# Kernel optimization log

Hardware: AMD Instinct MI355X
Metric: run time of the kernel (lower is better)

## Reference

```python
import jax, jax.numpy as jnp
import numpy as np

N_QUBITS = 22


def setup_inputs() -> dict:
    n = N_QUBITS
    dim = 2 ** n
    key = jax.random.key(0)
    k1, k2, k3, k4, k5 = jax.random.split(key, 5)
    return {
        "state_real": jax.random.normal(k1, (dim,), jnp.float32),
        "state_imag": jax.random.normal(k2, (dim,), jnp.float32),
        "rabi": jax.random.uniform(k3, (1,), jnp.float32),
        "detune": jax.random.uniform(k4, (1,), jnp.float32),
        "U": jax.random.normal(k5, (n, n), jnp.float32),
        "n_qubits": n,
    }


def reference(state_real, state_imag, rabi, detune, U, n_qubits):
    """kron_sum of H_rabi (Pauli-X per qubit, weight rabi/2), diagonal detune
    (weight -detune per qubit) and diagonal pairwise interaction (triu(U,1)),
    applied to a 2**n complex state vector."""
    n = n_qubits
    dim = 2 ** n
    psi = (state_real + 1j * state_imag).astype(jnp.complex64).reshape((2,) * n)

    # parse_weights: per-qubit rabi/2 for X terms, -detune for number operators
    w_x = jnp.full((n,), rabi[0] * 0.5)
    w_d = jnp.full((n,), -detune[0])

    # sum_k (rabi/2) * X_k |psi>  : X_k flips qubit-k axis of the state tensor
    x_acc = jnp.zeros_like(psi)
    for k in range(n):  # fixed small structural loop over qubits
        x_acc = x_acc + w_x[k] * jnp.flip(psi, axis=k)

    # bit table: bits[k, b] = k-th qubit bit of basis index b (axis 0 = MSB)
    basis = jnp.arange(dim, dtype=jnp.uint32)
    shifts = jnp.arange(n - 1, -1, -1, dtype=jnp.uint32)
    bits = ((basis[None, :] >> shifts[:, None]) & 1).astype(jnp.float32)  # [n, 2**n]

    # diagonal one-body detune: sum_k w_d[k] * bit_k
    diag_one = jnp.einsum("k,kn->n", w_d, bits)
    # diagonal two-body interaction: sum_{i<j} U[i,j] * bit_i * bit_j
    Ut = jnp.triu(U, k=1)
    diag_two = jnp.sum((Ut @ bits) * bits, axis=0)

    diag = (diag_one + diag_two).reshape((2,) * n)
    out = (x_acc + diag * psi).reshape(dim)
    return jnp.stack([out.real, out.imag])  # [2, 2**n] (real, imag)
```

## Files before the change

kernel.cpp:

```cpp
#include <hip/hip_runtime.h>

#define NQ 22
#define DIM (1 << NQ)
#define TILE 2048
#define LOG_TILE 11

typedef float f32x4_t __attribute__((ext_vector_type(4)));

__global__ __launch_bounds__(256) void ryd_precompute_B(const float* __restrict__ U,
                                                        float* __restrict__ Btab) {
    int t = blockIdx.x * blockDim.x + threadIdx.x;
    __shared__ float Us[NQ * NQ];
    for (int i = threadIdx.x; i < NQ * NQ; i += blockDim.x) Us[i] = U[i];
    __syncthreads();
    float b = 0.f;
    #pragma unroll
    for (int p = 1; p <= 10; ++p) {
        if ((t >> p) & 1) {
            #pragma unroll
            for (int q = 0; q < p; ++q) {
                if ((t >> q) & 1) b += Us[(21 - p) * NQ + (21 - q)];
            }
        }
    }
    Btab[t] = b;
}

#define ACC8(a0, a1, b0, b1)                                              \
    do {                                                                  \
        ar[0] += (a0).x; ar[1] += (a0).y; ar[2] += (a0).z; ar[3] += (a0).w; \
        ar[4] += (a1).x; ar[5] += (a1).y; ar[6] += (a1).z; ar[7] += (a1).w; \
        ai[0] += (b0).x; ai[1] += (b0).y; ai[2] += (b0).z; ai[3] += (b0).w; \
        ai[4] += (b1).x; ai[5] += (b1).y; ai[6] += (b1).z; ai[7] += (b1).w; \
    } while (0)

__device__ __forceinline__ int swz(int c) { return c ^ ((c >> 3) & 1); }

__global__ __launch_bounds__(256) void ryd_rows(
    const float* __restrict__ sr_g, const float* __restrict__ si_g,
    const float* __restrict__ rabi, const float* __restrict__ detune,
    const float* __restrict__ U, const float* __restrict__ Btab,
    float* __restrict__ out) {
    __shared__ float4 srv[TILE / 4];
    __shared__ float4 siv[TILE / 4];
    __shared__ float AD[12];

    const int h = blockIdx.x;
    const int tid = threadIdx.x;
    const int m0 = tid << 3;
    const int base = h << LOG_TILE;

    float4 r0 = *(const float4*)(sr_g + base + m0);
    float4 r1 = *(const float4*)(sr_g + base + m0 + 4);
    float4 i0 = *(const float4*)(si_g + base + m0);
    float4 i1 = *(const float4*)(si_g + base + m0 + 4);

    float4 B0 = *(const float4*)(Btab + m0);
    float4 B1 = *(const float4*)(Btab + m0 + 4);

    srv[swz(2 * tid)]     = r0;
    srv[swz(2 * tid + 1)] = r1;
    siv[swz(2 * tid)]     = i0;
    siv[swz(2 * tid + 1)] = i1;

    if (tid < 11) {
        int q = tid;
        float d = 0.f;
        #pragma unroll
        for (int hp = 0; hp <= 10; ++hp)
            if ((h >> hp) & 1) d += U[(10 - hp) * NQ + (21 - q)];
        AD[q] = d;
    } else if (tid == 11) {
        float a = 0.f;
        #pragma unroll
        for (int hp = 1; hp <= 10; ++hp) {
            if ((h >> hp) & 1) {
                #pragma unroll
                for (int hq = 0; hq < hp; ++hq)
                    if ((h >> hq) & 1) a += U[(10 - hp) * NQ + (10 - hq)];
            }
        }
        AD[11] = a;
    }

    float pr[8]  = {r0.x, r0.y, r0.z, r0.w, r1.x, r1.y, r1.z, r1.w};
    float pi_[8] = {i0.x, i0.y, i0.z, i0.w, i1.x, i1.y, i1.z, i1.w};

    __syncthreads();

    float ar[8], ai[8];
    #pragma unroll
    for (int e = 0; e < 8; ++e) {
        ar[e] = pr[e ^ 1] + pr[e ^ 2] + pr[e ^ 4];
        ai[e] = pi_[e ^ 1] + pi_[e ^ 2] + pi_[e ^ 4];
    }

    #pragma unroll
    for (int jj = 0; jj < 8; ++jj) {
        int p = tid ^ (1 << jj);
        float4 a0 = srv[swz(2 * p)];
        float4 a1 = srv[swz(2 * p + 1)];
        float4 b0 = siv[swz(2 * p)];
        float4 b1 = siv[swz(2 * p + 1)];
        ACC8(a0, a1, b0, b1);
    }

    const float det = detune[0];
    const float hrabi = 0.5f * rabi[0];
    float Dq0 = AD[0] - det;
    float Dq1 = AD[1] - det;
    float Dq2 = AD[2] - det;
    float diagBase = AD[11] - det * (float)__popc((unsigned)h);
    #pragma unroll
    for (int j = 0; j < 8; ++j)
        if ((tid >> j) & 1) diagBase += AD[j + 3] - det;

    float Bv[8] = {B0.x, B0.y, B0.z, B0.w, B1.x, B1.y, B1.z, B1.w};

    float orv[8], oiv[8];
    #pragma unroll
    for (int e = 0; e < 8; ++e) {
        float d = diagBase + Bv[e];
        if (e & 1) d += Dq0;
        if (e & 2) d += Dq1;
        if (e & 4) d += Dq2;
        orv[e] = hrabi * ar[e] + d * pr[e];
        oiv[e] = hrabi * ai[e] + d * pi_[e];
    }

    f32x4_t o0 = {orv[0], orv[1], orv[2], orv[3]};
    f32x4_t o1 = {orv[4], orv[5], orv[6], orv[7]};
    f32x4_t o2 = {oiv[0], oiv[1], oiv[2], oiv[3]};
    f32x4_t o3 = {oiv[4], oiv[5], oiv[6], oiv[7]};
    __builtin_nontemporal_store(o0, (f32x4_t*)(out + base + m0));
    __builtin_nontemporal_store(o1, (f32x4_t*)(out + base + m0 + 4));
    __builtin_nontemporal_store(o2, (f32x4_t*)(out + DIM + base + m0));
    __builtin_nontemporal_store(o3, (f32x4_t*)(out + DIM + base + m0 + 4));
}

__global__ __launch_bounds__(1024, 4) void ryd_cols(
    const float* __restrict__ sr_g, const float* __restrict__ si_g,
    const float* __restrict__ rabi, float* __restrict__ out) {
    __shared__ f32x4_t L[TILE * 4];

    const int b = blockIdx.x;
    const int A = b & 1;
    const int C0 = (b >> 1) << 4;
    const float* __restrict__ src = A ? si_g : sr_g;
    float* __restrict__ dst = out + (A ? DIM : 0);
    const int t = threadIdx.x;
    const float hrabi = 0.5f * rabi[0];

    #pragma unroll
    for (int k = 0; k < 8; ++k) {
        int n = t + (k << 10);
        int r = n >> 2, cv = n & 3;
        L[(r << 2) + cv] = *(const f32x4_t*)(src + (r << 11) + C0 + (cv << 2));
    }

    f32x4_t cur[8];
    #pragma unroll
    for (int k = 0; k < 8; ++k) {
        int n = t + (k << 10);
        int r = n >> 2, cv = n & 3;
        cur[k] = __builtin_nontemporal_load(
            (const f32x4_t*)(dst + (r << 11) + C0 + (cv << 2)));
    }

    __syncthreads();

    #pragma unroll
    for (int k = 0; k < 8; ++k) {
        int n = t + (k << 10);
        int r = n >> 2, cv = n & 3;
        f32x4_t acc = L[((r ^ 1) << 2) + cv];
        #pragma unroll
        for (int j = 1; j < 11; ++j)
            acc += L[(((r ^ (1 << j)) << 2)) + cv];
        f32x4_t res = cur[k] + acc * hrabi;
        __builtin_nontemporal_store(res, (f32x4_t*)(dst + (r << 11) + C0 + (cv << 2)));
    }
}

extern "C" void kernel_launch(void* const* d_in, const int* in_sizes, int n_in,
                              void* d_out, int out_size, void* d_ws, size_t ws_size,
                              hipStream_t stream) {
    const float* state_real = (const float*)d_in[0];
    const float* state_imag = (const float*)d_in[1];
    const float* rabi       = (const float*)d_in[2];
    const float* detune     = (const float*)d_in[3];
    const float* U          = (const float*)d_in[4];
    float* Btab = (float*)d_ws;
    float* out  = (float*)d_out;

    ryd_precompute_B<<<TILE / 256, 256, 0, stream>>>(U, Btab);
    ryd_rows<<<DIM / TILE, 256, 0, stream>>>(state_real, state_imag, rabi, detune,
                                             U, Btab, out);
    ryd_cols<<<256, 1024, 0, stream>>>(state_real, state_imag, rabi, out);
}
```

Before: 132.6 us.

## Run column-flip pass first with half-height tiles, then accumulate in row pass

The column kernel (high-qubit flips) now runs before the row kernel and writes partial results. The row kernel reads those partials and adds its own terms. Each column block covers only 1024 rows, taking the top-bit partner directly from global memory, which doubles the block count and halves shared memory per block. This aims to raise occupancy and parallelism in the column pass at the cost of extra global reads of the partner half-tile.

```diff
diff --git a/kernel.cpp b/kernel.cpp
--- a/kernel.cpp
+++ b/kernel.cpp
@@ -35,6 +35,53 @@
     } while (0)
 
 __device__ __forceinline__ int swz(int c) { return c ^ ((c >> 3) & 1); }
+
+__global__ __launch_bounds__(512, 4) void ryd_cols(
+    const float* __restrict__ sr_g, const float* __restrict__ si_g,
+    const float* __restrict__ rabi, float* __restrict__ out) {
+    __shared__ f32x4_t L[1024 * 4];
+
+    const int b = blockIdx.x;
+    const int A = b & 1;
+    const int half = (b >> 1) & 1;
+    const int C0 = (b >> 2) << 4;
+    const int R0 = half << 10;
+    const float* __restrict__ src = A ? si_g : sr_g;
+    float* __restrict__ dst = out + (A ? DIM : 0);
+    const int t = threadIdx.x;
+    const float hrabi = 0.5f * rabi[0];
+
+    #pragma unroll
+    for (int k = 0; k < 8; ++k) {
+        int n = t + (k << 9);
+        int r = n >> 2, cv = n & 3;
+        L[(r << 2) + cv] =
+            *(const f32x4_t*)(src + ((R0 + r) << 11) + C0 + (cv << 2));
+    }
+
+    f32x4_t pp[8];
+    #pragma unroll
+    for (int k = 0; k < 8; ++k) {
+        int n = t + (k << 9);
+        int r = n >> 2, cv = n & 3;
+        pp[k] = *(const f32x4_t*)(src + (((R0 ^ 1024) + r) << 11) + C0 + (cv << 2));
+    }
+
+    __syncthreads();
+
+    #pragma unroll
+    for (int k = 0; k < 8; ++k) {
+        int n = t + (k << 9);
+        int r = n >> 2, cv = n & 3;
+        f32x4_t acc = pp[k];
+        #pragma unroll
+        for (int j = 0; j < 10; ++j)
+            acc += L[((r ^ (1 << j)) << 2) + cv];
+        f32x4_t res = acc * hrabi;
+        __builtin_nontemporal_store(
+            res, (f32x4_t*)(dst + ((R0 + r) << 11) + C0 + (cv << 2)));
+    }
+}
 
 __global__ __launch_bounds__(256) void ryd_rows(
     const float* __restrict__ sr_g, const float* __restrict__ si_g,
@@ -57,6 +104,11 @@
 
     float4 B0 = *(const float4*)(Btab + m0);
     float4 B1 = *(const float4*)(Btab + m0 + 4);
+
+    float4 z0 = *(const float4*)(out + base + m0);
+    float4 z1 = *(const float4*)(out + base + m0 + 4);
+    float4 z2 = *(const float4*)(out + DIM + base + m0);
+    float4 z3 = *(const float4*)(out + DIM + base + m0 + 4);
 
     srv[swz(2 * tid)]     = r0;
     srv[swz(2 * tid + 1)] = r1;
@@ -116,6 +168,8 @@
         if ((tid >> j) & 1) diagBase += AD[j + 3] - det;
 
     float Bv[8] = {B0.x, B0.y, B0.z, B0.w, B1.x, B1.y, B1.z, B1.w};
+    float zr[8] = {z0.x, z0.y, z0.z, z0.w, z1.x, z1.y, z1.z, z1.w};
+    float zi[8] = {z2.x, z2.y, z2.z, z2.w, z3.x, z3.y, z3.z, z3.w};
 
     float orv[8], oiv[8];
     #pragma unroll
@@ -124,8 +178,8 @@
         if (e & 1) d += Dq0;
         if (e & 2) d += Dq1;
         if (e & 4) d += Dq2;
-        orv[e] = hrabi * ar[e] + d * pr[e];
-        oiv[e] = hrabi * ai[e] + d * pi_[e];
+        orv[e] = zr[e] + hrabi * ar[e] + d * pr[e];
+        oiv[e] = zi[e] + hrabi * ai[e] + d * pi_[e];
     }
 
     f32x4_t o0 = {orv[0], orv[1], orv[2], orv[3]};
@@ -136,50 +190,6 @@
     __builtin_nontemporal_store(o1, (f32x4_t*)(out + base + m0 + 4));
     __builtin_nontemporal_store(o2, (f32x4_t*)(out + DIM + base + m0));
     __builtin_nontemporal_store(o3, (f32x4_t*)(out + DIM + base + m0 + 4));
-}
-
-__global__ __launch_bounds__(1024, 4) void ryd_cols(
-    const float* __restrict__ sr_g, const float* __restrict__ si_g,
-    const float* __restrict__ rabi, float* __restrict__ out) {
-    __shared__ f32x4_t L[TILE * 4];
-
-    const int b = blockIdx.x;
-    const int A = b & 1;
-    const int C0 = (b >> 1) << 4;
-    const float* __restrict__ src = A ? si_g : sr_g;
-    float* __restrict__ dst = out + (A ? DIM : 0);
-    const int t = threadIdx.x;
-    const float hrabi = 0.5f * rabi[0];
-
-    #pragma unroll
-    for (int k = 0; k < 8; ++k) {
-        int n = t + (k << 10);
-        int r = n >> 2, cv = n & 3;
-        L[(r << 2) + cv] = *(const f32x4_t*)(src + (r << 11) + C0 + (cv << 2));
-    }
-
-    f32x4_t cur[8];
-    #pragma unroll
-    for (int k = 0; k < 8; ++k) {
-        int n = t + (k << 10);
-        int r = n >> 2, cv = n & 3;
-        cur[k] = __builtin_nontemporal_load(
-            (const f32x4_t*)(dst + (r << 11) + C0 + (cv << 2)));
-    }
-
-    __syncthreads();
-
-    #pragma unroll
-    for (int k = 0; k < 8; ++k) {
-        int n = t + (k << 10);
-        int r = n >> 2, cv = n & 3;
-        f32x4_t acc = L[((r ^ 1) << 2) + cv];
-        #pragma unroll
-        for (int j = 1; j < 11; ++j)
-            acc += L[(((r ^ (1 << j)) << 2)) + cv];
-        f32x4_t res = cur[k] + acc * hrabi;
-        __builtin_nontemporal_store(res, (f32x4_t*)(dst + (r << 11) + C0 + (cv << 2)));
-    }
 }
 
 extern "C" void kernel_launch(void* const* d_in, const int* in_sizes, int n_in,
@@ -194,7 +204,7 @@
     float* out  = (float*)d_out;
 
     ryd_precompute_B<<<TILE / 256, 256, 0, stream>>>(U, Btab);
+    ryd_cols<<<512, 512, 0, stream>>>(state_real, state_imag, rabi, out);
     ryd_rows<<<DIM / TILE, 256, 0, stream>>>(state_real, state_imag, rabi, detune,
                                              U, Btab, out);
-    ryd_cols<<<256, 1024, 0, stream>>>(state_real, state_imag, rabi, out);
-}
+}
```

New measurement: 131.6 us. About the same (-0.7%).
